# Optimization experiments

Hardware: AMD Instinct MI355X
Metric: run time of the kernel (lower is better)

The kernel has to match this reference:

```python
import jax, jax.numpy as jnp
import numpy as np

ST_RATIO = 1.5  # slice-thickness / in-plane-resolution ratio (module init arg)


def setup_inputs() -> dict:
    key = jax.random.key(0)
    k1, k2 = jax.random.split(key)
    B, H, W, D, S = 8, 160, 160, 96, 64
    vol = jax.random.normal(k1, (B, H, W, D, 1), dtype=jnp.float32)
    # small perturbations around identity (identity row is added inside reference)
    trf = jax.random.normal(k2, (B, S, 12), dtype=jnp.float32) * 0.05
    return {"vol": vol, "trf": trf}


def _trilinear(v, loc):
    """v: [H, W, D] volume; loc: [..., 3] float sample locations (voxel coords).
    Border-clipped trilinear interpolation (as in neuron's interpn)."""
    H, W, D = v.shape
    maxs_f = jnp.asarray([H - 1, W - 1, D - 1], dtype=loc.dtype)
    loc = jnp.clip(loc, 0.0, maxs_f)
    f = jnp.floor(loc)
    d = loc - f  # fractional part, in [0, 1)
    i0 = f.astype(jnp.int32)
    i1 = jnp.minimum(i0 + 1, jnp.asarray([H - 1, W - 1, D - 1], dtype=jnp.int32))
    out = jnp.zeros(loc.shape[:-1], dtype=v.dtype)
    for cx in (0, 1):
        for cy in (0, 1):
            for cz in (0, 1):
                ix = i1[..., 0] if cx else i0[..., 0]
                iy = i1[..., 1] if cy else i0[..., 1]
                iz = i1[..., 2] if cz else i0[..., 2]
                w = ((d[..., 0] if cx else 1.0 - d[..., 0])
                     * (d[..., 1] if cy else 1.0 - d[..., 1])
                     * (d[..., 2] if cz else 1.0 - d[..., 2]))
                out = out + w * v[ix, iy, iz]
    return out


def reference(vol, trf):
    """Volume-to-slice resampling.
    vol: [B, H, W, D, 1]; trf: [B, S, 12] per-slice affine params (flattened 3x4).
    Identity row added per original: trf += eye(4)[:3, :].
    Output: [B, H, W, S, 1]."""
    B, H, W, D, _ = vol.shape
    S = trf.shape[1]
    A = trf.reshape(B, S, 3, 4) + jnp.eye(4, dtype=trf.dtype)[:3, :]  # [B,S,3,4]

    # slice-plane sampling grid: in-plane (i, j) over HxW, through-plane z = s * st_ratio
    ii, jj = jnp.meshgrid(jnp.arange(H, dtype=jnp.float32),
                          jnp.arange(W, dtype=jnp.float32), indexing="ij")
    zz = jnp.arange(S, dtype=jnp.float32) * ST_RATIO
    ones = jnp.ones((S, H, W), dtype=jnp.float32)
    grid = jnp.stack([ii[None] * ones, jj[None] * ones,
                      zz[:, None, None] * ones, ones], axis=-1)  # [S,H,W,4] homogeneous

    loc = jnp.einsum("bsij,shwj->bshwi", A, grid)  # [B,S,H,W,3] volume coords
    out = jax.vmap(_trilinear)(vol[..., 0], loc)    # [B,S,H,W]
    return jnp.transpose(out, (0, 2, 3, 1))[..., None]  # [B,H,W,S,1]
```

## Files before the change

### kernel.cpp

```cpp
#include <hip/hip_runtime.h>
#include <hip/hip_fp16.h>

#define B 8
#define H 160
#define W 160
#define D 96
#define S 64
#define ST_RATIO 1.5f

__global__ __launch_bounds__(256) void v2s_transpose(
    const float* __restrict__ vol, __half* __restrict__ volT)
{
    __shared__ float t[32][33];
    const int blk = blockIdx.x;
    const int bh  = blk / 15;
    const int rem = blk - bh * 15;
    const int wt  = rem / 3;
    const int dt  = rem - wt * 3;
    const float* in  = vol  + (size_t)bh * (W * D);
    __half*      op  = volT + (size_t)bh * (D * W);
    const int tx = threadIdx.x & 31, ty = threadIdx.x >> 5;
#pragma unroll
    for (int r = 0; r < 4; ++r) {
        const int w_ = wt * 32 + ty + 8 * r;
        const int d_ = dt * 32 + tx;
        t[ty + 8 * r][tx] = in[w_ * D + d_];
    }
    __syncthreads();
#pragma unroll
    for (int r = 0; r < 4; ++r) {
        const int d_ = dt * 32 + ty + 8 * r;
        const int w_ = wt * 32 + tx;
        op[d_ * W + w_] = __float2half(t[tx][ty + 8 * r]);
    }
}

__global__ __launch_bounds__(256) void v2s_main(
    const __half* __restrict__ volT,
    const float*  __restrict__ trf,
    float*        __restrict__ out)
{
    __shared__ float As[S * 12];
    __shared__ float outT[64][65];

    const int bid  = blockIdx.x;
    const int tile = (bid & 7) * 400 + (bid >> 3);
    const int b    = tile / 400;
    const int hw0  = (tile - b * 400) * 64;

    const float* tb = trf + (size_t)b * (S * 12);
    for (int e = threadIdx.x; e < S * 12; e += 256) {
        const int j = e % 12;
        float v = tb[e];
        if ((j & 3) == (j >> 2)) v += 1.0f;
        As[e] = v;
    }
    __syncthreads();

    const int lane = threadIdx.x & 63;
    const int wid  = threadIdx.x >> 6;
    const int hw   = hw0 + lane;
    const int h    = hw / W;
    const int w    = hw - h * W;
    const float fh = (float)h, fw = (float)w;
    const __half* vb = volT + (size_t)b * (H * D * W);

#pragma unroll 4
    for (int it = 0; it < 16; ++it) {
        const int s = it * 4 + wid;
        const float* a = &As[s * 12];
        const float fz = (float)s * ST_RATIO;

        float x = fmaf(a[0], fh, fmaf(a[1], fw, fmaf(a[2],  fz, a[3])));
        float y = fmaf(a[4], fh, fmaf(a[5], fw, fmaf(a[6],  fz, a[7])));
        float z = fmaf(a[8], fh, fmaf(a[9], fw, fmaf(a[10], fz, a[11])));

        x = fminf(fmaxf(x, 0.0f), (float)(H - 1));
        y = fminf(fmaxf(y, 0.0f), (float)(W - 1));
        z = fminf(fmaxf(z, 0.0f), (float)(D - 1));

        const float flx = floorf(x), fly = floorf(y), flz = floorf(z);
        const float dx = x - flx, dy = y - fly, dz = z - flz;
        const int ix0 = (int)flx, iy0 = (int)fly, iz0 = (int)flz;
        const int ix1 = min(ix0 + 1, H - 1);
        const int iy1 = min(iy0 + 1, W - 1);
        const int iz1 = min(iz0 + 1, D - 1);

        const __half* p00 = vb + (ix0 * D + iz0) * W;
        const __half* p01 = vb + (ix0 * D + iz1) * W;
        const __half* p10 = vb + (ix1 * D + iz0) * W;
        const __half* p11 = vb + (ix1 * D + iz1) * W;

        const float v000 = __half2float(p00[iy0]), v001 = __half2float(p00[iy1]);
        const float v010 = __half2float(p01[iy0]), v011 = __half2float(p01[iy1]);
        const float v100 = __half2float(p10[iy0]), v101 = __half2float(p10[iy1]);
        const float v110 = __half2float(p11[iy0]), v111 = __half2float(p11[iy1]);

        const float c00 = fmaf(dy, v001 - v000, v000);
        const float c01 = fmaf(dy, v011 - v010, v010);
        const float c10 = fmaf(dy, v101 - v100, v100);
        const float c11 = fmaf(dy, v111 - v110, v110);
        const float c0  = fmaf(dz, c01 - c00, c00);
        const float c1  = fmaf(dz, c11 - c10, c10);
        outT[lane][s]   = fmaf(dx, c1 - c0, c0);
    }
    __syncthreads();

    const int s_out = lane;
#pragma unroll
    for (int r = 0; r < 16; ++r) {
        const int hw_off = wid + 4 * r;
        out[((size_t)(b * (H * W) + hw0 + hw_off)) * S + s_out] = outT[hw_off][s_out];
    }
}

__global__ __launch_bounds__(256) void v2s_fallback(
    const float* __restrict__ vol, const float* __restrict__ trf,
    float* __restrict__ out)
{
    __shared__ float As[S * 13];
    const int pos0 = blockIdx.x * 4;
    const int b = pos0 / (H * W);
    const float* tb = trf + (size_t)b * S * 12;
    for (int e = threadIdx.x; e < S * 12; e += 256) {
        int s = e / 12, j = e - s * 12;
        float v = tb[e];
        if ((j & 3) == (j >> 2)) v += 1.0f;
        As[s * 13 + j] = v;
    }
    __syncthreads();
    const int s   = threadIdx.x & 63;
    const int pos = pos0 + (threadIdx.x >> 6);
    const int hw  = pos % (H * W);
    const int h   = hw / W;
    const int w   = hw - h * W;
    const float* a = &As[s * 13];
    const float fh = (float)h, fw = (float)w, fz = (float)s * ST_RATIO;
    float x = fmaf(a[0], fh, fmaf(a[1], fw, fmaf(a[2],  fz, a[3])));
    float y = fmaf(a[4], fh, fmaf(a[5], fw, fmaf(a[6],  fz, a[7])));
    float z = fmaf(a[8], fh, fmaf(a[9], fw, fmaf(a[10], fz, a[11])));
    x = fminf(fmaxf(x, 0.0f), (float)(H - 1));
    y = fminf(fmaxf(y, 0.0f), (float)(W - 1));
    z = fminf(fmaxf(z, 0.0f), (float)(D - 1));
    const float flx = floorf(x), fly = floorf(y), flz = floorf(z);
    const float dx = x - flx, dy = y - fly, dz = z - flz;
    const int ix0 = (int)flx, iy0 = (int)fly, iz0 = (int)flz;
    const int ix1 = min(ix0 + 1, H - 1);
    const int iy1 = min(iy0 + 1, W - 1);
    const int iz1 = min(iz0 + 1, D - 1);
    const float* vb  = vol + (size_t)b * (H * W * D);
    const float* p00 = vb + (ix0 * W + iy0) * D;
    const float* p01 = vb + (ix0 * W + iy1) * D;
    const float* p10 = vb + (ix1 * W + iy0) * D;
    const float* p11 = vb + (ix1 * W + iy1) * D;
    const float v000 = p00[iz0], v001 = p00[iz1];
    const float v010 = p01[iz0], v011 = p01[iz1];
    const float v100 = p10[iz0], v101 = p10[iz1];
    const float v110 = p11[iz0], v111 = p11[iz1];
    const float c00 = fmaf(dz, v001 - v000, v000);
    const float c01 = fmaf(dz, v011 - v010, v010);
    const float c10 = fmaf(dz, v101 - v100, v100);
    const float c11 = fmaf(dz, v111 - v110, v110);
    const float c0  = fmaf(dy, c01 - c00, c00);
    const float c1  = fmaf(dy, c11 - c10, c10);
    out[(size_t)pos * S + s] = fmaf(dx, c1 - c0, c0);
}

extern "C" void kernel_launch(void* const* d_in, const int* in_sizes, int n_in,
                              void* d_out, int out_size, void* d_ws, size_t ws_size,
                              hipStream_t stream) {
    const float* vol = (const float*)d_in[0];
    const float* trf = (const float*)d_in[1];
    float* out = (float*)d_out;

    const size_t volT_bytes = (size_t)B * H * D * W * sizeof(__half);
    if (ws_size >= volT_bytes) {
        __half* volT = (__half*)d_ws;
        v2s_transpose<<<B * H * 5 * 3, 256, 0, stream>>>(vol, volT);
        v2s_main<<<(B * H * W) / 64, 256, 0, stream>>>(volT, trf, out);
    } else {
        v2s_fallback<<<(B * H * W) / 4, 256, 0, stream>>>(vol, trf, out);
    }
}
```

Baseline: 188.1 us.

## Pre-pack y/z neighbor quads so each sample needs two 8-byte gathers

Adds a prep kernel that converts the volume to half precision and stores, for every (x,z,y) voxel, its four y/z neighbours packed as a ushort4. The main kernel then does two 8-byte gathers per sample instead of eight 2-byte gathers. This cuts the number of scattered memory requests, but the prep pass writes a buffer four times larger than the transposed half-precision one, which adds write and read traffic. The path runs only when the workspace is large enough for the packed buffer; otherwise the old transpose path or the fallback is used.

```diff
diff --git a/kernel.cpp b/kernel.cpp
--- a/kernel.cpp
+++ b/kernel.cpp
@@ -7,6 +7,115 @@
 #define D 96
 #define S 64
 #define ST_RATIO 1.5f
+
+__global__ __launch_bounds__(256) void v2s_quadprep(
+    const float* __restrict__ vol, ushort4* __restrict__ volQ)
+{
+    __shared__ __half ph[W * 106];
+    const int bh = blockIdx.x;
+    const float* in = vol + (size_t)bh * (W * D);
+
+    for (int idx = threadIdx.x; idx < W * (D / 4); idx += 256) {
+        const int w_ = idx / (D / 4), k = idx - w_ * (D / 4);
+        const float4 f = *(const float4*)(in + w_ * D + 4 * k);
+        __half2* dst = (__half2*)&ph[w_ * 106 + 4 * k];
+        dst[0] = __floats2half2_rn(f.x, f.y);
+        dst[1] = __floats2half2_rn(f.z, f.w);
+    }
+    __syncthreads();
+
+    ushort4* op = volQ + (size_t)bh * (D * W);
+    for (int idx = threadIdx.x; idx < D * W; idx += 256) {
+        const int d_ = idx / W, w_ = idx - d_ * W;
+        const int w1 = min(w_ + 1, W - 1), d1 = min(d_ + 1, D - 1);
+        ushort4 q;
+        q.x = __half_as_ushort(ph[w_ * 106 + d_]);
+        q.y = __half_as_ushort(ph[w1 * 106 + d_]);
+        q.z = __half_as_ushort(ph[w_ * 106 + d1]);
+        q.w = __half_as_ushort(ph[w1 * 106 + d1]);
+        op[idx] = q;
+    }
+}
+
+__global__ __launch_bounds__(256) void v2s_main_q(
+    const ushort4* __restrict__ volQ,
+    const float*  __restrict__ trf,
+    float*        __restrict__ out)
+{
+    __shared__ float As[S * 12];
+    __shared__ float outT[64][65];
+
+    const int bid  = blockIdx.x;
+    const int tile = (bid & 7) * 400 + (bid >> 3);
+    const int b    = tile / 400;
+    const int hw0  = (tile - b * 400) * 64;
+
+    const float* tb = trf + (size_t)b * (S * 12);
+    for (int e = threadIdx.x; e < S * 12; e += 256) {
+        const int j = e % 12;
+        float v = tb[e];
+        if ((j & 3) == (j >> 2)) v += 1.0f;
+        As[e] = v;
+    }
+    __syncthreads();
+
+    const int lane = threadIdx.x & 63;
+    const int wid  = threadIdx.x >> 6;
+    const int hw   = hw0 + lane;
+    const int h    = hw / W;
+    const int w    = hw - h * W;
+    const float fh = (float)h, fw = (float)w;
+    const ushort4* vb = volQ + (size_t)b * (H * D * W);
+
+#pragma unroll 4
+    for (int it = 0; it < 16; ++it) {
+        const int s = it * 4 + wid;
+        const float* a = &As[s * 12];
+        const float fz = (float)s * ST_RATIO;
+
+        float x = fmaf(a[0], fh, fmaf(a[1], fw, fmaf(a[2],  fz, a[3])));
+        float y = fmaf(a[4], fh, fmaf(a[5], fw, fmaf(a[6],  fz, a[7])));
+        float z = fmaf(a[8], fh, fmaf(a[9], fw, fmaf(a[10], fz, a[11])));
+
+        x = fminf(fmaxf(x, 0.0f), (float)(H - 1));
+        y = fminf(fmaxf(y, 0.0f), (float)(W - 1));
+        z = fminf(fmaxf(z, 0.0f), (float)(D - 1));
+
+        const float flx = floorf(x), fly = floorf(y), flz = floorf(z);
+        const float dx = x - flx, dy = y - fly, dz = z - flz;
+        const int ix0 = (int)flx, iy0 = (int)fly, iz0 = (int)flz;
+        const int ix1 = min(ix0 + 1, H - 1);
+
+        const int base = iz0 * W + iy0;
+        const ushort4 q0 = vb[ix0 * (D * W) + base];
+        const ushort4 q1 = vb[ix1 * (D * W) + base];
+
+        const float q0y0z0 = __half2float(__ushort_as_half(q0.x));
+        const float q0y1z0 = __half2float(__ushort_as_half(q0.y));
+        const float q0y0z1 = __half2float(__ushort_as_half(q0.z));
+        const float q0y1z1 = __half2float(__ushort_as_half(q0.w));
+        const float q1y0z0 = __half2float(__ushort_as_half(q1.x));
+        const float q1y1z0 = __half2float(__ushort_as_half(q1.y));
+        const float q1y0z1 = __half2float(__ushort_as_half(q1.z));
+        const float q1y1z1 = __half2float(__ushort_as_half(q1.w));
+
+        const float a00 = fmaf(dy, q0y1z0 - q0y0z0, q0y0z0);
+        const float a01 = fmaf(dy, q0y1z1 - q0y0z1, q0y0z1);
+        const float a10 = fmaf(dy, q1y1z0 - q1y0z0, q1y0z0);
+        const float a11 = fmaf(dy, q1y1z1 - q1y0z1, q1y0z1);
+        const float e0  = fmaf(dz, a01 - a00, a00);
+        const float e1  = fmaf(dz, a11 - a10, a10);
+        outT[lane][s]   = fmaf(dx, e1 - e0, e0);
+    }
+    __syncthreads();
+
+    const int s_out = lane;
+#pragma unroll
+    for (int r = 0; r < 16; ++r) {
+        const int hw_off = wid + 4 * r;
+        out[((size_t)(b * (H * W) + hw0 + hw_off)) * S + s_out] = outT[hw_off][s_out];
+    }
+}
 
 __global__ __launch_bounds__(256) void v2s_transpose(
     const float* __restrict__ vol, __half* __restrict__ volT)
@@ -22,32 +131,25 @@
     const int tx = threadIdx.x & 31, ty = threadIdx.x >> 5;
 #pragma unroll
     for (int r = 0; r < 4; ++r) {
-        const int w_ = wt * 32 + ty + 8 * r;
-        const int d_ = dt * 32 + tx;
-        t[ty + 8 * r][tx] = in[w_ * D + d_];
+        t[ty + 8 * r][tx] = in[(wt * 32 + ty + 8 * r) * D + dt * 32 + tx];
     }
     __syncthreads();
 #pragma unroll
     for (int r = 0; r < 4; ++r) {
-        const int d_ = dt * 32 + ty + 8 * r;
-        const int w_ = wt * 32 + tx;
-        op[d_ * W + w_] = __float2half(t[tx][ty + 8 * r]);
+        op[(dt * 32 + ty + 8 * r) * W + wt * 32 + tx] = __float2half(t[tx][ty + 8 * r]);
     }
 }
 
 __global__ __launch_bounds__(256) void v2s_main(
-    const __half* __restrict__ volT,
-    const float*  __restrict__ trf,
-    float*        __restrict__ out)
+    const __half* __restrict__ volT, const float* __restrict__ trf,
+    float* __restrict__ out)
 {
     __shared__ float As[S * 12];
     __shared__ float outT[64][65];
-
     const int bid  = blockIdx.x;
     const int tile = (bid & 7) * 400 + (bid >> 3);
     const int b    = tile / 400;
     const int hw0  = (tile - b * 400) * 64;
-
     const float* tb = trf + (size_t)b * (S * 12);
     for (int e = threadIdx.x; e < S * 12; e += 256) {
         const int j = e % 12;
@@ -56,7 +158,6 @@
         As[e] = v;
     }
     __syncthreads();
-
     const int lane = threadIdx.x & 63;
     const int wid  = threadIdx.x >> 6;
     const int hw   = hw0 + lane;
@@ -64,38 +165,31 @@
     const int w    = hw - h * W;
     const float fh = (float)h, fw = (float)w;
     const __half* vb = volT + (size_t)b * (H * D * W);
-
 #pragma unroll 4
     for (int it = 0; it < 16; ++it) {
         const int s = it * 4 + wid;
         const float* a = &As[s * 12];
         const float fz = (float)s * ST_RATIO;
-
         float x = fmaf(a[0], fh, fmaf(a[1], fw, fmaf(a[2],  fz, a[3])));
         float y = fmaf(a[4], fh, fmaf(a[5], fw, fmaf(a[6],  fz, a[7])));
         float z = fmaf(a[8], fh, fmaf(a[9], fw, fmaf(a[10], fz, a[11])));
-
         x = fminf(fmaxf(x, 0.0f), (float)(H - 1));
         y = fminf(fmaxf(y, 0.0f), (float)(W - 1));
         z = fminf(fmaxf(z, 0.0f), (float)(D - 1));
-
         const float flx = floorf(x), fly = floorf(y), flz = floorf(z);
         const float dx = x - flx, dy = y - fly, dz = z - flz;
         const int ix0 = (int)flx, iy0 = (int)fly, iz0 = (int)flz;
         const int ix1 = min(ix0 + 1, H - 1);
         const int iy1 = min(iy0 + 1, W - 1);
         const int iz1 = min(iz0 + 1, D - 1);
-
         const __half* p00 = vb + (ix0 * D + iz0) * W;
         const __half* p01 = vb + (ix0 * D + iz1) * W;
         const __half* p10 = vb + (ix1 * D + iz0) * W;
         const __half* p11 = vb + (ix1 * D + iz1) * W;
-
         const float v000 = __half2float(p00[iy0]), v001 = __half2float(p00[iy1]);
         const float v010 = __half2float(p01[iy0]), v011 = __half2float(p01[iy1]);
         const float v100 = __half2float(p10[iy0]), v101 = __half2float(p10[iy1]);
         const float v110 = __half2float(p11[iy0]), v111 = __half2float(p11[iy1]);
-
         const float c00 = fmaf(dy, v001 - v000, v000);
         const float c01 = fmaf(dy, v011 - v010, v010);
         const float c10 = fmaf(dy, v101 - v100, v100);
@@ -105,7 +199,6 @@
         outT[lane][s]   = fmaf(dx, c1 - c0, c0);
     }
     __syncthreads();
-
     const int s_out = lane;
 #pragma unroll
     for (int r = 0; r < 16; ++r) {
@@ -173,8 +266,13 @@
     const float* trf = (const float*)d_in[1];
     float* out = (float*)d_out;
 
+    const size_t quad_bytes = (size_t)B * H * D * W * sizeof(ushort4);
     const size_t volT_bytes = (size_t)B * H * D * W * sizeof(__half);
-    if (ws_size >= volT_bytes) {
+    if (ws_size >= quad_bytes) {
+        ushort4* volQ = (ushort4*)d_ws;
+        v2s_quadprep<<<B * H, 256, 0, stream>>>(vol, volQ);
+        v2s_main_q<<<(B * H * W) / 64, 256, 0, stream>>>(volQ, trf, out);
+    } else if (ws_size >= volT_bytes) {
         __half* volT = (__half*)d_ws;
         v2s_transpose<<<B * H * 5 * 3, 256, 0, stream>>>(vol, volT);
         v2s_main<<<(B * H * W) / 64, 256, 0, stream>>>(volT, trf, out);
```

Result: slower. 208.5 us (+10.8%).

## Vectorize transpose prep and write outputs directly as float4 per thread

Applied to the files above, without the earlier changes.

The transpose kernel now loads whole D rows with float4, converts to half in shared memory and writes half2 pairs, using one block per 32-column strip instead of 32x32 tiles. The main kernel drops the shared-memory output transpose and barrier. Each thread computes 4 consecutive slices and stores them as a float4. Blocks now cover 128 positions, with warps split over pixel halves and slice halves. The float4 stores are strided by S per lane, so coalescing may be worse than the old transposed stores, in exchange for less shared memory and no sync.

```diff
diff --git a/kernel.cpp b/kernel.cpp
--- a/kernel.cpp
+++ b/kernel.cpp
@@ -8,45 +8,45 @@
 #define S 64
 #define ST_RATIO 1.5f
 
-__global__ __launch_bounds__(256) void v2s_transpose(
+__global__ __launch_bounds__(256) void v2s_prep(
     const float* __restrict__ vol, __half* __restrict__ volT)
 {
-    __shared__ float t[32][33];
+    __shared__ __half ph[32][98];
     const int blk = blockIdx.x;
-    const int bh  = blk / 15;
-    const int rem = blk - bh * 15;
-    const int wt  = rem / 3;
-    const int dt  = rem - wt * 3;
-    const float* in  = vol  + (size_t)bh * (W * D);
-    __half*      op  = volT + (size_t)bh * (D * W);
-    const int tx = threadIdx.x & 31, ty = threadIdx.x >> 5;
-#pragma unroll
-    for (int r = 0; r < 4; ++r) {
-        const int w_ = wt * 32 + ty + 8 * r;
-        const int d_ = dt * 32 + tx;
-        t[ty + 8 * r][tx] = in[w_ * D + d_];
+    const int bh  = blk / 5;
+    const int w0  = (blk - bh * 5) * 32;
+    const float* in = vol + ((size_t)bh * W + w0) * D;
+
+    for (int i = threadIdx.x; i < 32 * 24; i += 256) {
+        const int wl = i / 24, k = i - wl * 24;
+        const float4 f = *(const float4*)(in + wl * D + 4 * k);
+        __half2* dst = (__half2*)&ph[wl][4 * k];
+        dst[0] = __floats2half2_rn(f.x, f.y);
+        dst[1] = __floats2half2_rn(f.z, f.w);
     }
     __syncthreads();
-#pragma unroll
-    for (int r = 0; r < 4; ++r) {
-        const int d_ = dt * 32 + ty + 8 * r;
-        const int w_ = wt * 32 + tx;
-        op[d_ * W + w_] = __float2half(t[tx][ty + 8 * r]);
+
+    __half* op = volT + (size_t)bh * (D * W) + w0;
+    for (int i = threadIdx.x; i < D * 16; i += 256) {
+        const int d = i >> 4, k = i & 15;
+        __half2 v;
+        v.x = ph[2 * k][d];
+        v.y = ph[2 * k + 1][d];
+        *(__half2*)(op + d * W + 2 * k) = v;
     }
 }
 
-__global__ __launch_bounds__(256) void v2s_main(
+__global__ __launch_bounds__(256) void v2s_main2(
     const __half* __restrict__ volT,
     const float*  __restrict__ trf,
     float*        __restrict__ out)
 {
     __shared__ float As[S * 12];
-    __shared__ float outT[64][65];
 
-    const int bid  = blockIdx.x;
-    const int tile = (bid & 7) * 400 + (bid >> 3);
-    const int b    = tile / 400;
-    const int hw0  = (tile - b * 400) * 64;
+    const int bid = blockIdx.x;
+    const int t   = (bid & 7) * 200 + (bid >> 3);
+    const int b   = t / 200;
+    const int hwb = (t - b * 200) * 128;
 
     const float* tb = trf + (size_t)b * (S * 12);
     for (int e = threadIdx.x; e < S * 12; e += 256) {
@@ -59,58 +59,59 @@
 
     const int lane = threadIdx.x & 63;
     const int wid  = threadIdx.x >> 6;
-    const int hw   = hw0 + lane;
+    const int hw   = hwb + (wid & 1) * 64 + lane;
+    const int sb0  = (wid >> 1) * 32;
     const int h    = hw / W;
     const int w    = hw - h * W;
     const float fh = (float)h, fw = (float)w;
     const __half* vb = volT + (size_t)b * (H * D * W);
+    float* ob = out + ((size_t)b * (H * W) + hw) * S;
 
-#pragma unroll 4
-    for (int it = 0; it < 16; ++it) {
-        const int s = it * 4 + wid;
-        const float* a = &As[s * 12];
-        const float fz = (float)s * ST_RATIO;
+    for (int it = 0; it < 8; ++it) {
+        const int s0 = sb0 + it * 4;
+        float res[4];
+#pragma unroll
+        for (int q = 0; q < 4; ++q) {
+            const int s = s0 + q;
+            const float* a = &As[s * 12];
+            const float fz = (float)s * ST_RATIO;
 
-        float x = fmaf(a[0], fh, fmaf(a[1], fw, fmaf(a[2],  fz, a[3])));
-        float y = fmaf(a[4], fh, fmaf(a[5], fw, fmaf(a[6],  fz, a[7])));
-        float z = fmaf(a[8], fh, fmaf(a[9], fw, fmaf(a[10], fz, a[11])));
+            float x = fmaf(a[0], fh, fmaf(a[1], fw, fmaf(a[2],  fz, a[3])));
+            float y = fmaf(a[4], fh, fmaf(a[5], fw, fmaf(a[6],  fz, a[7])));
+            float z = fmaf(a[8], fh, fmaf(a[9], fw, fmaf(a[10], fz, a[11])));
 
-        x = fminf(fmaxf(x, 0.0f), (float)(H - 1));
-        y = fminf(fmaxf(y, 0.0f), (float)(W - 1));
-        z = fminf(fmaxf(z, 0.0f), (float)(D - 1));
+            x = fminf(fmaxf(x, 0.0f), (float)(H - 1));
+            y = fminf(fmaxf(y, 0.0f), (float)(W - 1));
+            z = fminf(fmaxf(z, 0.0f), (float)(D - 1));
 
-        const float flx = floorf(x), fly = floorf(y), flz = floorf(z);
-        const float dx = x - flx, dy = y - fly, dz = z - flz;
-        const int ix0 = (int)flx, iy0 = (int)fly, iz0 = (int)flz;
-        const int ix1 = min(ix0 + 1, H - 1);
-        const int iy1 = min(iy0 + 1, W - 1);
-        const int iz1 = min(iz0 + 1, D - 1);
+            const float flx = floorf(x), fly = floorf(y), flz = floorf(z);
+            const float dx = x - flx, dy = y - fly, dz = z - flz;
+            const int ix0 = (int)flx, iy0 = (int)fly, iz0 = (int)flz;
+            const int ix1 = min(ix0 + 1, H - 1);
+            const int iy1 = min(iy0 + 1, W - 1);
+            const int iz1 = min(iz0 + 1, D - 1);
 
-        const __half* p00 = vb + (ix0 * D + iz0) * W;
-        const __half* p01 = vb + (ix0 * D + iz1) * W;
-        const __half* p10 = vb + (ix1 * D + iz0) * W;
-        const __half* p11 = vb + (ix1 * D + iz1) * W;
+            const __half* p00 = vb + (ix0 * D + iz0) * W;
+            const __half* p01 = vb + (ix0 * D + iz1) * W;
+            const __half* p10 = vb + (ix1 * D + iz0) * W;
+            const __half* p11 = vb + (ix1 * D + iz1) * W;
 
-        const float v000 = __half2float(p00[iy0]), v001 = __half2float(p00[iy1]);
-        const float v010 = __half2float(p01[iy0]), v011 = __half2float(p01[iy1]);
-        const float v100 = __half2float(p10[iy0]), v101 = __half2float(p10[iy1]);
-        const float v110 = __half2float(p11[iy0]), v111 = __half2float(p11[iy1]);
+            const float v000 = __half2float(p00[iy0]), v001 = __half2float(p00[iy1]);
+            const float v010 = __half2float(p01[iy0]), v011 = __half2float(p01[iy1]);
+            const float v100 = __half2float(p10[iy0]), v101 = __half2float(p10[iy1]);
+            const float v110 = __half2float(p11[iy0]), v111 = __half2float(p11[iy1]);
 
-        const float c00 = fmaf(dy, v001 - v000, v000);
-        const float c01 = fmaf(dy, v011 - v010, v010);
-        const float c10 = fmaf(dy, v101 - v100, v100);
-        const float c11 = fmaf(dy, v111 - v110, v110);
-        const float c0  = fmaf(dz, c01 - c00, c00);
-        const float c1  = fmaf(dz, c11 - c10, c10);
-        outT[lane][s]   = fmaf(dx, c1 - c0, c0);
-    }
-    __syncthreads();
-
-    const int s_out = lane;
-#pragma unroll
-    for (int r = 0; r < 16; ++r) {
-        const int hw_off = wid + 4 * r;
-        out[((size_t)(b * (H * W) + hw0 + hw_off)) * S + s_out] = outT[hw_off][s_out];
+            const float c00 = fmaf(dy, v001 - v000, v000);
+            const float c01 = fmaf(dy, v011 - v010, v010);
+            const float c10 = fmaf(dy, v101 - v100, v100);
+            const float c11 = fmaf(dy, v111 - v110, v110);
+            const float c0  = fmaf(dz, c01 - c00, c00);
+            const float c1  = fmaf(dz, c11 - c10, c10);
+            res[q] = fmaf(dx, c1 - c0, c0);
+        }
+        float4 v4;
+        v4.x = res[0]; v4.y = res[1]; v4.z = res[2]; v4.w = res[3];
+        *(float4*)(ob + s0) = v4;
     }
 }
 
@@ -176,8 +177,8 @@
     const size_t volT_bytes = (size_t)B * H * D * W * sizeof(__half);
     if (ws_size >= volT_bytes) {
         __half* volT = (__half*)d_ws;
-        v2s_transpose<<<B * H * 5 * 3, 256, 0, stream>>>(vol, volT);
-        v2s_main<<<(B * H * W) / 64, 256, 0, stream>>>(volT, trf, out);
+        v2s_prep<<<B * H * 5, 256, 0, stream>>>(vol, volT);
+        v2s_main2<<<1600, 256, 0, stream>>>(volT, trf, out);
     } else {
         v2s_fallback<<<(B * H * W) / 4, 256, 0, stream>>>(vol, trf, out);
     }
```

After: 241.7 us. 1.28x slower.

## Restructure transpose to whole-row float4 loads and read affine params directly

Applied to the files above, without the earlier changes.

The transpose kernel now processes an entire (b,h) W×D slab per 512-thread block, loading with float4, converting to half in shared memory, and writing half2 pairs. The main kernel drops the shared-memory staging of affine parameters and its barrier, reading trf directly (wave-uniform loads) and folding the identity term into the coordinate computation. This targets transpose memory efficiency and removes a synchronization and shared traffic in the main kernel. In exchange the transpose uses a large shared tile (about 34 KB), which limits occupancy, and its strided shared reads of half values may hit bank conflicts.

```diff
diff --git a/kernel.cpp b/kernel.cpp
--- a/kernel.cpp
+++ b/kernel.cpp
@@ -8,54 +8,43 @@
 #define S 64
 #define ST_RATIO 1.5f
 
-__global__ __launch_bounds__(256) void v2s_transpose(
+__global__ __launch_bounds__(512) void v2s_prep2(
     const float* __restrict__ vol, __half* __restrict__ volT)
 {
-    __shared__ float t[32][33];
-    const int blk = blockIdx.x;
-    const int bh  = blk / 15;
-    const int rem = blk - bh * 15;
-    const int wt  = rem / 3;
-    const int dt  = rem - wt * 3;
-    const float* in  = vol  + (size_t)bh * (W * D);
-    __half*      op  = volT + (size_t)bh * (D * W);
-    const int tx = threadIdx.x & 31, ty = threadIdx.x >> 5;
-#pragma unroll
-    for (int r = 0; r < 4; ++r) {
-        const int w_ = wt * 32 + ty + 8 * r;
-        const int d_ = dt * 32 + tx;
-        t[ty + 8 * r][tx] = in[w_ * D + d_];
+    __shared__ __half ph[W * 106];
+    const int bh = blockIdx.x;
+    const float* in = vol + (size_t)bh * (W * D);
+
+    for (int i = threadIdx.x; i < W * (D / 4); i += 512) {
+        const int w_ = i / 24, k = i - w_ * 24;
+        const float4 f = *(const float4*)(in + w_ * D + 4 * k);
+        __half2* dst = (__half2*)&ph[w_ * 106 + 4 * k];
+        dst[0] = __floats2half2_rn(f.x, f.y);
+        dst[1] = __floats2half2_rn(f.z, f.w);
     }
     __syncthreads();
-#pragma unroll
-    for (int r = 0; r < 4; ++r) {
-        const int d_ = dt * 32 + ty + 8 * r;
-        const int w_ = wt * 32 + tx;
-        op[d_ * W + w_] = __float2half(t[tx][ty + 8 * r]);
+
+    __half* op = volT + (size_t)bh * (D * W);
+    for (int i = threadIdx.x; i < D * (W / 2); i += 512) {
+        const int d = i / 80, k = i - d * 80;
+        __half2 v;
+        v.x = ph[(2 * k) * 106 + d];
+        v.y = ph[(2 * k + 1) * 106 + d];
+        *(__half2*)(op + d * W + 2 * k) = v;
     }
 }
 
-__global__ __launch_bounds__(256) void v2s_main(
+__global__ __launch_bounds__(256) void v2s_main3(
     const __half* __restrict__ volT,
     const float*  __restrict__ trf,
     float*        __restrict__ out)
 {
-    __shared__ float As[S * 12];
     __shared__ float outT[64][65];
 
     const int bid  = blockIdx.x;
     const int tile = (bid & 7) * 400 + (bid >> 3);
     const int b    = tile / 400;
     const int hw0  = (tile - b * 400) * 64;
-
-    const float* tb = trf + (size_t)b * (S * 12);
-    for (int e = threadIdx.x; e < S * 12; e += 256) {
-        const int j = e % 12;
-        float v = tb[e];
-        if ((j & 3) == (j >> 2)) v += 1.0f;
-        As[e] = v;
-    }
-    __syncthreads();
 
     const int lane = threadIdx.x & 63;
     const int wid  = threadIdx.x >> 6;
@@ -64,16 +53,17 @@
     const int w    = hw - h * W;
     const float fh = (float)h, fw = (float)w;
     const __half* vb = volT + (size_t)b * (H * D * W);
+    const float* tb  = trf + (size_t)b * (S * 12);
 
 #pragma unroll 4
     for (int it = 0; it < 16; ++it) {
         const int s = it * 4 + wid;
-        const float* a = &As[s * 12];
+        const float* a = tb + s * 12;
         const float fz = (float)s * ST_RATIO;
 
-        float x = fmaf(a[0], fh, fmaf(a[1], fw, fmaf(a[2],  fz, a[3])));
-        float y = fmaf(a[4], fh, fmaf(a[5], fw, fmaf(a[6],  fz, a[7])));
-        float z = fmaf(a[8], fh, fmaf(a[9], fw, fmaf(a[10], fz, a[11])));
+        float x = fh + fmaf(a[0], fh, fmaf(a[1], fw, fmaf(a[2],  fz, a[3])));
+        float y = fw + fmaf(a[4], fh, fmaf(a[5], fw, fmaf(a[6],  fz, a[7])));
+        float z = fz + fmaf(a[8], fh, fmaf(a[9], fw, fmaf(a[10], fz, a[11])));
 
         x = fminf(fmaxf(x, 0.0f), (float)(H - 1));
         y = fminf(fmaxf(y, 0.0f), (float)(W - 1));
@@ -176,8 +166,8 @@
     const size_t volT_bytes = (size_t)B * H * D * W * sizeof(__half);
     if (ws_size >= volT_bytes) {
         __half* volT = (__half*)d_ws;
-        v2s_transpose<<<B * H * 5 * 3, 256, 0, stream>>>(vol, volT);
-        v2s_main<<<(B * H * W) / 64, 256, 0, stream>>>(volT, trf, out);
+        v2s_prep2<<<B * H, 512, 0, stream>>>(vol, volT);
+        v2s_main3<<<3200, 256, 0, stream>>>(volT, trf, out);
     } else {
         v2s_fallback<<<(B * H * W) / 4, 256, 0, stream>>>(vol, trf, out);
     }
```

New measurement: 207.3 us. 1.1x slower.
